# Optimization experiments

Measured on AMD Instinct MI355X. Metric: run time of the kernel, lower is better.

Reference implementation:

```python
import jax, jax.numpy as jnp
import numpy as np

GAMMA = -0.1
XI = 1.1
I, J = 4096, 4096
NP0, NP1 = 10, 10


def setup_inputs() -> dict:
    key = jax.random.key(0)
    k1, k2, k3, k4, k5, k6 = jax.random.split(key, 6)
    weight = jax.random.normal(k1, (I, J), dtype=jnp.float32)
    sparse_mask = jax.random.uniform(k2, (I, J), dtype=jnp.float32, minval=-1.0, maxval=1.0)
    permutation_scales0 = jax.random.normal(k3, (NP0, I), dtype=jnp.float32) / NP0
    permutation_scales1 = jax.random.normal(k4, (NP1, J), dtype=jnp.float32) / NP1
    # first row is identity permutation, rest are random permutations (as in torch init)
    p0 = [jnp.arange(I, dtype=jnp.int32)] + [jax.random.permutation(jax.random.fold_in(k5, t), I).astype(jnp.int32) for t in range(NP0 - 1)]
    p1 = [jnp.arange(J, dtype=jnp.int32)] + [jax.random.permutation(jax.random.fold_in(k6, t), J).astype(jnp.int32) for t in range(NP1 - 1)]
    permutations0 = jnp.stack(p0)  # (NP0, I)
    permutations1 = jnp.stack(p1)  # (NP1, J)
    return {
        "weight": weight,
        "sparse_mask": sparse_mask,
        "permutation_scales0": permutation_scales0,
        "permutation_scales1": permutation_scales1,
        "permutations0": permutations0,
        "permutations1": permutations1,
    }


def _soft_mask(sparse_mask):
    # clip((xi - gamma) * sigmoid(x) + gamma, 0, 1)
    return jnp.clip((XI - GAMMA) * jax.nn.sigmoid(sparse_mask) + GAMMA, 0.0, 1.0)


def reference(weight, sparse_mask, permutation_scales0, permutation_scales1, permutations0, permutations1):
    sparse_weight = weight * _soft_mask(sparse_mask)  # (I, J)
    # gather permuted columns: (I, NP1, J), combine with per-(perm, col) scales -> (I, J)
    w = jnp.einsum("ipj,pj->ij", sparse_weight[:, permutations1], permutation_scales1)
    # gather permuted rows: (NP0, I, J), combine with per-(perm, row) scales -> (I, J)
    w = jnp.einsum("pij,pi->ij", w[permutations0, :], permutation_scales0)
    return w
```

## Files before the change

### kernel.cpp

```cpp
#include <hip/hip_runtime.h>
#include <hip/hip_bf16.h>

#define I_DIM 4096
#define J_DIM 4096
#define NPERM0 10
#define NPERM1 10
#define RROWS 4
#define CHUNKS 8
#define CCOLS (J_DIM / CHUNKS)
#define K2_ROWS 16

typedef float          f32x4 __attribute__((ext_vector_type(4)));
typedef int            i32x4 __attribute__((ext_vector_type(4)));
typedef unsigned short u16x4 __attribute__((ext_vector_type(4)));
typedef unsigned short u16x8 __attribute__((ext_vector_type(8)));

__device__ __forceinline__ int swzB(int s) { return s ^ ((s >> 4) & 7); }

__device__ __forceinline__ float bf2f(unsigned short u) {
    return __uint_as_float((unsigned)u << 16);
}
__device__ __forceinline__ unsigned short f2bf(float f) {
    unsigned u = __float_as_uint(f);
    u += 0x7FFFu + ((u >> 16) & 1u);
    return (unsigned short)(u >> 16);
}

__device__ __forceinline__ float soft_mask(float x) {
    float s = 1.0f / (1.0f + __expf(-x));
    return fminf(fmaxf(1.2f * s - 0.1f, 0.0f), 1.0f);
}

__global__ __launch_bounds__(512, 4) void maskcolmix_kernel(
    const float* __restrict__ w,
    const float* __restrict__ m,
    const float* __restrict__ ps1,
    const int*   __restrict__ perm1,
    unsigned short* __restrict__ ub) {
    __shared__ u16x4 vlds[J_DIM];

    const int i0 = blockIdx.x * RROWS;
    const int c8 = threadIdx.x;

    u16x8 rowv[RROWS];
#pragma unroll
    for (int r = 0; r < RROWS; ++r) {
        const f32x4* w4 = reinterpret_cast<const f32x4*>(
                              w + (size_t)(i0 + r) * J_DIM) + 2 * c8;
        const f32x4* m4 = reinterpret_cast<const f32x4*>(
                              m + (size_t)(i0 + r) * J_DIM) + 2 * c8;
        f32x4 w0 = __builtin_nontemporal_load(w4);
        f32x4 w1 = __builtin_nontemporal_load(w4 + 1);
        f32x4 m0 = __builtin_nontemporal_load(m4);
        f32x4 m1 = __builtin_nontemporal_load(m4 + 1);
        u16x8 o;
#pragma unroll
        for (int k = 0; k < 4; ++k) {
            o[k]     = f2bf(w0[k] * soft_mask(m0[k]));
            o[k + 4] = f2bf(w1[k] * soft_mask(m1[k]));
        }
        rowv[r] = o;
    }
#pragma unroll
    for (int k = 0; k < 8; ++k) {
        u16x4 t;
#pragma unroll
        for (int r = 0; r < RROWS; ++r) t[r] = rowv[r][k];
        vlds[swzB(8 * c8 + k)] = t;
    }
    __syncthreads();

    float o[RROWS][8];
#pragma unroll
    for (int r = 0; r < RROWS; ++r)
#pragma unroll
        for (int k = 0; k < 8; ++k) o[r][k] = 0.f;

#pragma unroll 2
    for (int q = 0; q < NPERM1; ++q) {
        const i32x4* pq = reinterpret_cast<const i32x4*>(perm1 + (size_t)q * J_DIM);
        const f32x4* sq = reinterpret_cast<const f32x4*>(ps1  + (size_t)q * J_DIM);
        i32x4 pc0 = pq[2 * c8];
        i32x4 pc1 = pq[2 * c8 + 1];
        f32x4 s0  = sq[2 * c8];
        f32x4 s1  = sq[2 * c8 + 1];
        u16x4 g[8];
#pragma unroll
        for (int k = 0; k < 4; ++k) {
            g[k]     = vlds[swzB(pc0[k])];
            g[k + 4] = vlds[swzB(pc1[k])];
        }
#pragma unroll
        for (int k = 0; k < 4; ++k) {
#pragma unroll
            for (int r = 0; r < RROWS; ++r) {
                o[r][k]     += s0[k] * bf2f(g[k][r]);
                o[r][k + 4] += s1[k] * bf2f(g[k + 4][r]);
            }
        }
    }
#pragma unroll
    for (int r = 0; r < RROWS; ++r) {
        u16x8 ob;
#pragma unroll
        for (int k = 0; k < 8; ++k) ob[k] = f2bf(o[r][k]);
        *reinterpret_cast<u16x8*>(ub + (size_t)(i0 + r) * J_DIM + (size_t)c8 * 8) = ob;
    }
}

__global__ __launch_bounds__(256, 4) void rowmix_out_kernel(
    const unsigned short* __restrict__ ub,
    const float* __restrict__ ps0,
    const int*   __restrict__ perm0,
    float* __restrict__ out) {
    const int chunk = blockIdx.x & (CHUNKS - 1);
    const int rg    = blockIdx.x / CHUNKS;
    const int wave  = threadIdx.x >> 6;
    const int lane  = threadIdx.x & 63;
    const int i0    = rg * K2_ROWS + wave * 4;
    const size_t colbase = (size_t)chunk * CCOLS + (size_t)lane * 8;

    float acc[4][8];
#pragma unroll
    for (int r = 0; r < 4; ++r)
#pragma unroll
        for (int k = 0; k < 8; ++k) acc[r][k] = 0.f;

#pragma unroll 2
    for (int p = 0; p < NPERM0; ++p) {
        u16x8 vv[4];
#pragma unroll
        for (int r = 0; r < 4; ++r) {
            int row = perm0[p * I_DIM + i0 + r];
            vv[r] = *reinterpret_cast<const u16x8*>(
                        ub + (size_t)row * J_DIM + colbase);
        }
#pragma unroll
        for (int r = 0; r < 4; ++r) {
            float s = ps0[p * I_DIM + i0 + r];
#pragma unroll
            for (int k = 0; k < 8; ++k) acc[r][k] += s * bf2f(vv[r][k]);
        }
    }
#pragma unroll
    for (int r = 0; r < 4; ++r) {
        f32x4 t0, t1;
#pragma unroll
        for (int k = 0; k < 4; ++k) { t0[k] = acc[r][k]; t1[k] = acc[r][k + 4]; }
        float* dst = out + (size_t)(i0 + r) * J_DIM + colbase;
        __builtin_nontemporal_store(t0, reinterpret_cast<f32x4*>(dst));
        __builtin_nontemporal_store(t1, reinterpret_cast<f32x4*>(dst) + 1);
    }
}

extern "C" void kernel_launch(void* const* d_in, const int* in_sizes, int n_in,
                              void* d_out, int out_size, void* d_ws, size_t ws_size,
                              hipStream_t stream) {
    const float* weight = (const float*)d_in[0];
    const float* smask  = (const float*)d_in[1];
    const float* ps0    = (const float*)d_in[2];
    const float* ps1    = (const float*)d_in[3];
    const int*   perm0  = (const int*)d_in[4];
    const int*   perm1  = (const int*)d_in[5];
    float* out = (float*)d_out;

    unsigned short* ub = (unsigned short*)d_ws;

    maskcolmix_kernel<<<I_DIM / RROWS, 512, 0, stream>>>(
        weight, smask, ps1, perm1, ub);
    rowmix_out_kernel<<<CHUNKS * (I_DIM / K2_ROWS), 256, 0, stream>>>(
        ub, ps0, perm0, out);
}
```

Before: 78.97 us.

## Process two row groups per block, prefetching second group's loads during gather

Each block of the mask/column-mix kernel now handles two 4-row groups and launches half as many blocks. While the first group's LDS gather runs, the global loads and soft-mask conversion for the second group are issued in two halves, hiding memory latency behind LDS work. The aim is to overlap HBM reads with the gather, at the cost of more registers and an extra LDS barrier round. The row-mix kernel's launch bounds also ask for higher occupancy (8 blocks per CU instead of 4).

```diff
diff --git a/kernel.cpp b/kernel.cpp
--- a/kernel.cpp
+++ b/kernel.cpp
@@ -31,6 +31,73 @@
     return fminf(fmaxf(1.2f * s - 0.1f, 0.0f), 1.0f);
 }
 
+__device__ __forceinline__ void issue_loads_2rows(
+    const float* __restrict__ w, const float* __restrict__ m,
+    int i, int c8, f32x4 pw[2][2], f32x4 pm[2][2]) {
+#pragma unroll
+    for (int r = 0; r < 2; ++r) {
+        const f32x4* w4 = reinterpret_cast<const f32x4*>(
+                              w + (size_t)(i + r) * J_DIM) + 2 * c8;
+        const f32x4* m4 = reinterpret_cast<const f32x4*>(
+                              m + (size_t)(i + r) * J_DIM) + 2 * c8;
+        pw[r][0] = __builtin_nontemporal_load(w4);
+        pw[r][1] = __builtin_nontemporal_load(w4 + 1);
+        pm[r][0] = __builtin_nontemporal_load(m4);
+        pm[r][1] = __builtin_nontemporal_load(m4 + 1);
+    }
+}
+
+__device__ __forceinline__ u16x8 conv_row(f32x4 w0, f32x4 w1, f32x4 m0, f32x4 m1) {
+    u16x8 o;
+#pragma unroll
+    for (int k = 0; k < 4; ++k) {
+        o[k]     = f2bf(w0[k] * soft_mask(m0[k]));
+        o[k + 4] = f2bf(w1[k] * soft_mask(m1[k]));
+    }
+    return o;
+}
+
+__device__ __forceinline__ void transpose_to_lds(u16x4* vlds, const u16x8 rowv[RROWS], int c8) {
+#pragma unroll
+    for (int k = 0; k < 8; ++k) {
+        u16x4 t;
+#pragma unroll
+        for (int r = 0; r < RROWS; ++r) t[r] = rowv[r][k];
+        vlds[swzB(8 * c8 + k)] = t;
+    }
+}
+
+template<int HALF>
+__device__ __forceinline__ void gather_half(
+    float (&o)[RROWS][8], const u16x4* vlds,
+    const int* __restrict__ perm1, const float* __restrict__ ps1, int c8) {
+    const int off = 2 * c8 + HALF;
+#pragma unroll 2
+    for (int q = 0; q < NPERM1; ++q) {
+        i32x4 pc = reinterpret_cast<const i32x4*>(perm1 + (size_t)q * J_DIM)[off];
+        f32x4 s  = reinterpret_cast<const f32x4*>(ps1  + (size_t)q * J_DIM)[off];
+        u16x4 g[4];
+#pragma unroll
+        for (int k = 0; k < 4; ++k) g[k] = vlds[swzB(pc[k])];
+#pragma unroll
+        for (int k = 0; k < 4; ++k)
+#pragma unroll
+            for (int r = 0; r < RROWS; ++r)
+                o[r][HALF * 4 + k] += s[k] * bf2f(g[k][r]);
+    }
+}
+
+__device__ __forceinline__ void store_u(
+    unsigned short* __restrict__ ub, int i, int c8, const float (&o)[RROWS][8]) {
+#pragma unroll
+    for (int r = 0; r < RROWS; ++r) {
+        u16x8 ob;
+#pragma unroll
+        for (int k = 0; k < 8; ++k) ob[k] = f2bf(o[r][k]);
+        *reinterpret_cast<u16x8*>(ub + (size_t)(i + r) * J_DIM + (size_t)c8 * 8) = ob;
+    }
+}
+
 __global__ __launch_bounds__(512, 4) void maskcolmix_kernel(
     const float* __restrict__ w,
     const float* __restrict__ m,
@@ -39,35 +106,21 @@
     unsigned short* __restrict__ ub) {
     __shared__ u16x4 vlds[J_DIM];
 
+    const int c8 = threadIdx.x;
     const int i0 = blockIdx.x * RROWS;
-    const int c8 = threadIdx.x;
+    const int i1 = (blockIdx.x + (int)gridDim.x) * RROWS;
 
     u16x8 rowv[RROWS];
-#pragma unroll
-    for (int r = 0; r < RROWS; ++r) {
-        const f32x4* w4 = reinterpret_cast<const f32x4*>(
-                              w + (size_t)(i0 + r) * J_DIM) + 2 * c8;
-        const f32x4* m4 = reinterpret_cast<const f32x4*>(
-                              m + (size_t)(i0 + r) * J_DIM) + 2 * c8;
-        f32x4 w0 = __builtin_nontemporal_load(w4);
-        f32x4 w1 = __builtin_nontemporal_load(w4 + 1);
-        f32x4 m0 = __builtin_nontemporal_load(m4);
-        f32x4 m1 = __builtin_nontemporal_load(m4 + 1);
-        u16x8 o;
-#pragma unroll
-        for (int k = 0; k < 4; ++k) {
-            o[k]     = f2bf(w0[k] * soft_mask(m0[k]));
-            o[k + 4] = f2bf(w1[k] * soft_mask(m1[k]));
-        }
-        rowv[r] = o;
-    }
-#pragma unroll
-    for (int k = 0; k < 8; ++k) {
-        u16x4 t;
-#pragma unroll
-        for (int r = 0; r < RROWS; ++r) t[r] = rowv[r][k];
-        vlds[swzB(8 * c8 + k)] = t;
-    }
+    {
+        f32x4 aw[2][2], am[2][2], bw[2][2], bm[2][2];
+        issue_loads_2rows(w, m, i0,     c8, aw, am);
+        issue_loads_2rows(w, m, i0 + 2, c8, bw, bm);
+        rowv[0] = conv_row(aw[0][0], aw[0][1], am[0][0], am[0][1]);
+        rowv[1] = conv_row(aw[1][0], aw[1][1], am[1][0], am[1][1]);
+        rowv[2] = conv_row(bw[0][0], bw[0][1], bm[0][0], bm[0][1]);
+        rowv[3] = conv_row(bw[1][0], bw[1][1], bm[1][0], bm[1][1]);
+    }
+    transpose_to_lds(vlds, rowv, c8);
     __syncthreads();
 
     float o[RROWS][8];
@@ -76,39 +129,31 @@
 #pragma unroll
         for (int k = 0; k < 8; ++k) o[r][k] = 0.f;
 
-#pragma unroll 2
-    for (int q = 0; q < NPERM1; ++q) {
-        const i32x4* pq = reinterpret_cast<const i32x4*>(perm1 + (size_t)q * J_DIM);
-        const f32x4* sq = reinterpret_cast<const f32x4*>(ps1  + (size_t)q * J_DIM);
-        i32x4 pc0 = pq[2 * c8];
-        i32x4 pc1 = pq[2 * c8 + 1];
-        f32x4 s0  = sq[2 * c8];
-        f32x4 s1  = sq[2 * c8 + 1];
-        u16x4 g[8];
-#pragma unroll
-        for (int k = 0; k < 4; ++k) {
-            g[k]     = vlds[swzB(pc0[k])];
-            g[k + 4] = vlds[swzB(pc1[k])];
-        }
-#pragma unroll
-        for (int k = 0; k < 4; ++k) {
-#pragma unroll
-            for (int r = 0; r < RROWS; ++r) {
-                o[r][k]     += s0[k] * bf2f(g[k][r]);
-                o[r][k + 4] += s1[k] * bf2f(g[k + 4][r]);
-            }
-        }
-    }
-#pragma unroll
-    for (int r = 0; r < RROWS; ++r) {
-        u16x8 ob;
-#pragma unroll
-        for (int k = 0; k < 8; ++k) ob[k] = f2bf(o[r][k]);
-        *reinterpret_cast<u16x8*>(ub + (size_t)(i0 + r) * J_DIM + (size_t)c8 * 8) = ob;
-    }
-}
-
-__global__ __launch_bounds__(256, 4) void rowmix_out_kernel(
+    f32x4 pw[2][2], pm[2][2];
+    issue_loads_2rows(w, m, i1, c8, pw, pm);
+    gather_half<0>(o, vlds, perm1, ps1, c8);
+    rowv[0] = conv_row(pw[0][0], pw[0][1], pm[0][0], pm[0][1]);
+    rowv[1] = conv_row(pw[1][0], pw[1][1], pm[1][0], pm[1][1]);
+    issue_loads_2rows(w, m, i1 + 2, c8, pw, pm);
+    gather_half<1>(o, vlds, perm1, ps1, c8);
+    rowv[2] = conv_row(pw[0][0], pw[0][1], pm[0][0], pm[0][1]);
+    rowv[3] = conv_row(pw[1][0], pw[1][1], pm[1][0], pm[1][1]);
+    store_u(ub, i0, c8, o);
+
+    __syncthreads();
+    transpose_to_lds(vlds, rowv, c8);
+    __syncthreads();
+
+#pragma unroll
+    for (int r = 0; r < RROWS; ++r)
+#pragma unroll
+        for (int k = 0; k < 8; ++k) o[r][k] = 0.f;
+    gather_half<0>(o, vlds, perm1, ps1, c8);
+    gather_half<1>(o, vlds, perm1, ps1, c8);
+    store_u(ub, i1, c8, o);
+}
+
+__global__ __launch_bounds__(256, 8) void rowmix_out_kernel(
     const unsigned short* __restrict__ ub,
     const float* __restrict__ ps0,
     const int*   __restrict__ perm0,
@@ -166,7 +211,7 @@
 
     unsigned short* ub = (unsigned short*)d_ws;
 
-    maskcolmix_kernel<<<I_DIM / RROWS, 512, 0, stream>>>(
+    maskcolmix_kernel<<<I_DIM / RROWS / 2, 512, 0, stream>>>(
         weight, smask, ps1, perm1, ub);
     rowmix_out_kernel<<<CHUNKS * (I_DIM / K2_ROWS), 256, 0, stream>>>(
         ub, ps0, perm0, out);
```

Result: slower. 103.6 us (+31.2%).
